# Kernel optimization log

Measured on AMD Instinct MI355X. Metric: run time of the kernel, lower is better.

The kernel has to match this reference:

```python
import jax, jax.numpy as jnp
import numpy as np

B, T, F, U = 64, 512, 1024, 64


def setup_inputs() -> dict:
    key = jax.random.key(0)
    ks = jax.random.split(key, 6)
    return {
        "x": jax.random.normal(ks[0], (B, T, F), dtype=jnp.float32),
        "kernel": jax.random.normal(ks[1], (F, U), dtype=jnp.float32) * (1.0 / np.sqrt(F)),
        "bias": jax.random.normal(ks[2], (U,), dtype=jnp.float32) * 0.02,
        "chain_kernel": jax.random.normal(ks[3], (U, U), dtype=jnp.float32) * 0.1,
        "left_boundary": jax.random.normal(ks[4], (U,), dtype=jnp.float32) * 0.1,
        "right_boundary": jax.random.normal(ks[5], (U,), dtype=jnp.float32) * 0.1,
    }


def _viterbi_decode(potentials, chain_kernel):
    # potentials: [B, T, U], chain_kernel: [U, U]
    def step(alpha, pot_t):
        # alpha: [B, U] best score ending in each tag at t-1
        scores = alpha[:, :, None] + chain_kernel[None, :, :] + pot_t[:, None, :]  # [B, U_prev, U_cur]
        return jnp.max(scores, axis=1), jnp.argmax(scores, axis=1)

    pots_t = jnp.moveaxis(potentials[:, 1:], 1, 0)  # [T-1, B, U]
    alpha_last, backptrs = jax.lax.scan(step, potentials[:, 0], pots_t)
    last_tag = jnp.argmax(alpha_last, axis=-1)  # [B]

    def back(tag, bp):
        prev = jnp.take_along_axis(bp, tag[:, None], axis=1)[:, 0]
        return prev, prev

    _, tags = jax.lax.scan(back, last_tag, backptrs, reverse=True)  # [T-1, B], positions 0..T-2
    path = jnp.concatenate([jnp.moveaxis(tags, 0, 1), last_tag[:, None]], axis=1)
    return path.astype(jnp.int32)


def reference(x, kernel, bias, chain_kernel, left_boundary, right_boundary):
    # dense projection (activation = linear)
    potentials = jnp.einsum("btf,fu->btu", x, kernel) + bias  # [B, T, U]
    # boundary energies (mask=None path: add to first/last timestep)
    potentials = potentials.at[:, 0, :].add(left_boundary)
    potentials = potentials.at[:, -1, :].add(right_boundary)
    return _viterbi_decode(potentials, chain_kernel)
```

## Files before the change

kernel.cpp:

```cpp
#include <hip/hip_runtime.h>

#define B_ 64
#define T_ 512
#define F_ 1024
#define U_ 64
#define FK 128
#define NCH (F_ / FK)

__global__ __launch_bounds__(256, 2) void crf_gemm_kernel(
    const float* __restrict__ x, const float* __restrict__ w,
    const float* __restrict__ bias, const float* __restrict__ lb,
    const float* __restrict__ rb, float* __restrict__ pot)
{
    __shared__ float wlds[FK * U_];

    const int tid = threadIdx.x;
    const int rt = tid >> 4;
    const int ut = tid & 15;
    const int n0 = blockIdx.x * 64;
    const int r0 = rt * 4;
    const int u0 = ut * 4;

    float acc[4][4];
#pragma unroll
    for (int i = 0; i < 4; ++i)
#pragma unroll
        for (int j = 0; j < 4; ++j) acc[i][j] = 0.f;

    const float* xrow = x + (size_t)(n0 + r0) * F_;

    float4 wst[8];
#pragma unroll
    for (int l = 0; l < 8; ++l)
        wst[l] = *reinterpret_cast<const float4*>(w + (size_t)(l * 256 + tid) * 4);
#pragma unroll
    for (int l = 0; l < 8; ++l)
        *reinterpret_cast<float4*>(&wlds[(l * 256 + tid) * 4]) = wst[l];
    __syncthreads();

    float4 xp0[4], xp1[4];
#pragma unroll
    for (int i = 0; i < 4; ++i)
        xp0[i] = *reinterpret_cast<const float4*>(xrow + (size_t)i * F_ + 0);
#pragma unroll
    for (int i = 0; i < 4; ++i)
        xp1[i] = *reinterpret_cast<const float4*>(xrow + (size_t)i * F_ + 4);

    for (int c = 0; c < NCH; ++c) {
        if (c + 1 < NCH) {
#pragma unroll
            for (int l = 0; l < 8; ++l)
                wst[l] = *reinterpret_cast<const float4*>(
                    w + (size_t)(c + 1) * (FK * U_) + (size_t)(l * 256 + tid) * 4);
        }

        float4 wc[4];
#pragma unroll
        for (int j = 0; j < 4; ++j)
            wc[j] = *reinterpret_cast<const float4*>(&wlds[(0 + j) * U_ + u0]);

        for (int kk = 0; kk < FK / 4; ++kk) {
            const int kg = (c * FK + kk * 4 + 8) & (F_ - 1);
            float4 xn[4];
#pragma unroll
            for (int i = 0; i < 4; ++i)
                xn[i] = *reinterpret_cast<const float4*>(xrow + (size_t)i * F_ + kg);

            float4 wn[4];
            const int krn = (kk * 4 + 4) & (FK - 1);
#pragma unroll
            for (int j = 0; j < 4; ++j)
                wn[j] = *reinterpret_cast<const float4*>(&wlds[(krn + j) * U_ + u0]);

#pragma unroll
            for (int ff = 0; ff < 4; ++ff) {
                const float4 wf = wc[ff];
#pragma unroll
                for (int i = 0; i < 4; ++i) {
                    const float xs = (ff == 0) ? xp0[i].x : (ff == 1) ? xp0[i].y
                                   : (ff == 2) ? xp0[i].z : xp0[i].w;
                    acc[i][0] = fmaf(xs, wf.x, acc[i][0]);
                    acc[i][1] = fmaf(xs, wf.y, acc[i][1]);
                    acc[i][2] = fmaf(xs, wf.z, acc[i][2]);
                    acc[i][3] = fmaf(xs, wf.w, acc[i][3]);
                }
            }
#pragma unroll
            for (int i = 0; i < 4; ++i) { xp0[i] = xp1[i]; xp1[i] = xn[i]; }
#pragma unroll
            for (int j = 0; j < 4; ++j) wc[j] = wn[j];
        }

        if (c + 1 < NCH) {
            __syncthreads();
#pragma unroll
            for (int l = 0; l < 8; ++l)
                *reinterpret_cast<float4*>(&wlds[(l * 256 + tid) * 4]) = wst[l];
            __syncthreads();
        }
    }

    const int t0 = n0 & (T_ - 1);
    const float4 bs4 = *reinterpret_cast<const float4*>(bias + u0);
    const float4 lb4 = *reinterpret_cast<const float4*>(lb + u0);
    const float4 rb4 = *reinterpret_cast<const float4*>(rb + u0);

#pragma unroll
    for (int i = 0; i < 4; ++i) {
        const int n = n0 + r0 + i;
        const int t = t0 + r0 + i;
        float4 o;
        o.x = acc[i][0] + bs4.x;
        o.y = acc[i][1] + bs4.y;
        o.z = acc[i][2] + bs4.z;
        o.w = acc[i][3] + bs4.w;
        if (t == 0)      { o.x += lb4.x; o.y += lb4.y; o.z += lb4.z; o.w += lb4.w; }
        if (t == T_ - 1) { o.x += rb4.x; o.y += rb4.y; o.z += rb4.z; o.w += rb4.w; }
        *reinterpret_cast<float4*>(pot + (size_t)n * U_ + u0) = o;
    }
}

__global__ __launch_bounds__(256) void crf_viterbi_kernel(
    const float* __restrict__ pot, const float* __restrict__ chain,
    int* __restrict__ path)
{
    const int b = blockIdx.x;
    const int tid = threadIdx.x;
    const int u = tid & 63;
    const int g = tid >> 6;

    __shared__ __align__(16) float alpha_s[64];
    __shared__ float pval[4][64];
    __shared__ int   pidx[4][64];
    __shared__ unsigned char bp[T_ - 1][64];
    __shared__ unsigned char cmap[4][64];
    __shared__ int es[4];

    float chain_r[16];
#pragma unroll
    for (int k = 0; k < 16; ++k)
        chain_r[k] = chain[(size_t)(g * 16 + k) * U_ + u];

    const float* potb = pot + (size_t)b * T_ * U_;

    if (g == 0) alpha_s[u] = potb[u];
    __syncthreads();

    float pc = potb[(size_t)U_ + u];

    for (int t = 1; t < T_; ++t) {
        const int tn = (t + 1 < T_) ? (t + 1) : (T_ - 1);
        const float pn = potb[(size_t)tn * U_ + u];

        const float4* a4 = reinterpret_cast<const float4*>(alpha_s);
        float best = -3.402823466e38f;
        int bidx = 0;
#pragma unroll
        for (int q = 0; q < 4; ++q) {
            const float4 av = a4[g * 4 + q];
            const float avv[4] = {av.x, av.y, av.z, av.w};
#pragma unroll
            for (int kk = 0; kk < 4; ++kk) {
                const int k = q * 4 + kk;
                const float s2 = (avv[kk] + chain_r[k]) + pc;
                if (s2 > best) { best = s2; bidx = g * 16 + k; }
            }
        }
        pval[g][u] = best;
        pidx[g][u] = bidx;
        __syncthreads();
        if (g == 0) {
            float bv = pval[0][u];
            int   bi = pidx[0][u];
#pragma unroll
            for (int j = 1; j < 4; ++j) {
                const float v = pval[j][u];
                if (v > bv) { bv = v; bi = pidx[j][u]; }
            }
            bp[t - 1][u] = (unsigned char)bi;
            alpha_s[u] = bv;
        }
        __syncthreads();
        pc = pn;
    }

    const int r0c = g * 128;
    const int r1c = (g == 3) ? (T_ - 1) : (g + 1) * 128;

    {
        int tag = u;
        for (int r = r1c - 1; r >= r0c; --r) tag = bp[r][tag];
        cmap[g][u] = (unsigned char)tag;
    }
    __syncthreads();

    if (tid == 0) {
        float bvv = alpha_s[0];
        int bii = 0;
        for (int v = 1; v < 64; ++v) {
            const float a = alpha_s[v];
            if (a > bvv) { bvv = a; bii = v; }
        }
        path[(size_t)b * T_ + (T_ - 1)] = bii;
        const int e3 = bii;
        const int e2 = cmap[3][e3];
        const int e1 = cmap[2][e2];
        const int e0 = cmap[1][e1];
        es[0] = e0; es[1] = e1; es[2] = e2; es[3] = e3;
    }
    __syncthreads();

    if (u == 0) {
        int tag = es[g];
        int* pb = path + (size_t)b * T_;
        for (int r = r1c - 1; r >= r0c; --r) {
            tag = bp[r][tag];
            pb[r] = tag;
        }
    }
}

extern "C" void kernel_launch(void* const* d_in, const int* in_sizes, int n_in,
                              void* d_out, int out_size, void* d_ws, size_t ws_size,
                              hipStream_t stream) {
    const float* x  = (const float*)d_in[0];
    const float* w  = (const float*)d_in[1];
    const float* bs = (const float*)d_in[2];
    const float* ck = (const float*)d_in[3];
    const float* lb = (const float*)d_in[4];
    const float* rb = (const float*)d_in[5];

    float* pot = (float*)d_ws;
    int* path  = (int*)d_out;

    crf_gemm_kernel<<<dim3(B_ * T_ / 64), dim3(256), 0, stream>>>(x, w, bs, lb, rb, pot);
    crf_viterbi_kernel<<<dim3(B_), dim3(256), 0, stream>>>(pot, ck, path);
}
```

Baseline: 344.5 us.

## Fuse projection GEMM into Viterbi kernel with producer waves computing potentials

Replaces the separate GEMM and Viterbi kernels with a single kernel of one 512-thread block per batch element. Four consumer waves run the Viterbi recurrence while four producer waves compute the next 64 timesteps of potentials into a double-buffered LDS tile, interleaved with each step's barriers. The intent is to remove the global round trip of the potentials and the standalone GEMM launch by hiding the projection behind the serial recurrence. In exchange, the GEMM now runs on only 64 blocks with no LDS reuse of the weights, and producer global-load latency can extend each barrier-bound Viterbi step.

Measured after the change: 757.0 us. +119.7%, slower.

```diff
diff --git a/kernel.cpp b/kernel.cpp
--- a/kernel.cpp
+++ b/kernel.cpp
@@ -4,131 +4,22 @@
 #define T_ 512
 #define F_ 1024
 #define U_ 64
-#define FK 128
-#define NCH (F_ / FK)
-
-__global__ __launch_bounds__(256, 2) void crf_gemm_kernel(
+
+__global__ __launch_bounds__(512) void crf_fused_kernel(
     const float* __restrict__ x, const float* __restrict__ w,
-    const float* __restrict__ bias, const float* __restrict__ lb,
-    const float* __restrict__ rb, float* __restrict__ pot)
-{
-    __shared__ float wlds[FK * U_];
-
-    const int tid = threadIdx.x;
-    const int rt = tid >> 4;
-    const int ut = tid & 15;
-    const int n0 = blockIdx.x * 64;
-    const int r0 = rt * 4;
-    const int u0 = ut * 4;
-
-    float acc[4][4];
-#pragma unroll
-    for (int i = 0; i < 4; ++i)
-#pragma unroll
-        for (int j = 0; j < 4; ++j) acc[i][j] = 0.f;
-
-    const float* xrow = x + (size_t)(n0 + r0) * F_;
-
-    float4 wst[8];
-#pragma unroll
-    for (int l = 0; l < 8; ++l)
-        wst[l] = *reinterpret_cast<const float4*>(w + (size_t)(l * 256 + tid) * 4);
-#pragma unroll
-    for (int l = 0; l < 8; ++l)
-        *reinterpret_cast<float4*>(&wlds[(l * 256 + tid) * 4]) = wst[l];
-    __syncthreads();
-
-    float4 xp0[4], xp1[4];
-#pragma unroll
-    for (int i = 0; i < 4; ++i)
-        xp0[i] = *reinterpret_cast<const float4*>(xrow + (size_t)i * F_ + 0);
-#pragma unroll
-    for (int i = 0; i < 4; ++i)
-        xp1[i] = *reinterpret_cast<const float4*>(xrow + (size_t)i * F_ + 4);
-
-    for (int c = 0; c < NCH; ++c) {
-        if (c + 1 < NCH) {
-#pragma unroll
-            for (int l = 0; l < 8; ++l)
-                wst[l] = *reinterpret_cast<const float4*>(
-                    w + (size_t)(c + 1) * (FK * U_) + (size_t)(l * 256 + tid) * 4);
-        }
-
-        float4 wc[4];
-#pragma unroll
-        for (int j = 0; j < 4; ++j)
-            wc[j] = *reinterpret_cast<const float4*>(&wlds[(0 + j) * U_ + u0]);
-
-        for (int kk = 0; kk < FK / 4; ++kk) {
-            const int kg = (c * FK + kk * 4 + 8) & (F_ - 1);
-            float4 xn[4];
-#pragma unroll
-            for (int i = 0; i < 4; ++i)
-                xn[i] = *reinterpret_cast<const float4*>(xrow + (size_t)i * F_ + kg);
-
-            float4 wn[4];
-            const int krn = (kk * 4 + 4) & (FK - 1);
-#pragma unroll
-            for (int j = 0; j < 4; ++j)
-                wn[j] = *reinterpret_cast<const float4*>(&wlds[(krn + j) * U_ + u0]);
-
-#pragma unroll
-            for (int ff = 0; ff < 4; ++ff) {
-                const float4 wf = wc[ff];
-#pragma unroll
-                for (int i = 0; i < 4; ++i) {
-                    const float xs = (ff == 0) ? xp0[i].x : (ff == 1) ? xp0[i].y
-                                   : (ff == 2) ? xp0[i].z : xp0[i].w;
-                    acc[i][0] = fmaf(xs, wf.x, acc[i][0]);
-                    acc[i][1] = fmaf(xs, wf.y, acc[i][1]);
-                    acc[i][2] = fmaf(xs, wf.z, acc[i][2]);
-                    acc[i][3] = fmaf(xs, wf.w, acc[i][3]);
-                }
-            }
-#pragma unroll
-            for (int i = 0; i < 4; ++i) { xp0[i] = xp1[i]; xp1[i] = xn[i]; }
-#pragma unroll
-            for (int j = 0; j < 4; ++j) wc[j] = wn[j];
-        }
-
-        if (c + 1 < NCH) {
-            __syncthreads();
-#pragma unroll
-            for (int l = 0; l < 8; ++l)
-                *reinterpret_cast<float4*>(&wlds[(l * 256 + tid) * 4]) = wst[l];
-            __syncthreads();
-        }
-    }
-
-    const int t0 = n0 & (T_ - 1);
-    const float4 bs4 = *reinterpret_cast<const float4*>(bias + u0);
-    const float4 lb4 = *reinterpret_cast<const float4*>(lb + u0);
-    const float4 rb4 = *reinterpret_cast<const float4*>(rb + u0);
-
-#pragma unroll
-    for (int i = 0; i < 4; ++i) {
-        const int n = n0 + r0 + i;
-        const int t = t0 + r0 + i;
-        float4 o;
-        o.x = acc[i][0] + bs4.x;
-        o.y = acc[i][1] + bs4.y;
-        o.z = acc[i][2] + bs4.z;
-        o.w = acc[i][3] + bs4.w;
-        if (t == 0)      { o.x += lb4.x; o.y += lb4.y; o.z += lb4.z; o.w += lb4.w; }
-        if (t == T_ - 1) { o.x += rb4.x; o.y += rb4.y; o.z += rb4.z; o.w += rb4.w; }
-        *reinterpret_cast<float4*>(pot + (size_t)n * U_ + u0) = o;
-    }
-}
-
-__global__ __launch_bounds__(256) void crf_viterbi_kernel(
-    const float* __restrict__ pot, const float* __restrict__ chain,
+    const float* __restrict__ bias, const float* __restrict__ chain,
+    const float* __restrict__ lb, const float* __restrict__ rb,
     int* __restrict__ path)
 {
     const int b = blockIdx.x;
     const int tid = threadIdx.x;
-    const int u = tid & 63;
-    const int g = tid >> 6;
-
+    const int lane = tid & 63;
+    const int wave = tid >> 6;
+    const bool cons = (wave < 4);
+    const int g = wave & 3;
+    const int u = lane;
+
+    __shared__ __align__(16) float potl[2][64][64];
     __shared__ __align__(16) float alpha_s[64];
     __shared__ float pval[4][64];
     __shared__ int   pidx[4][64];
@@ -136,61 +27,200 @@
     __shared__ unsigned char cmap[4][64];
     __shared__ int es[4];
 
+    {
+        const int rt = tid >> 4;
+        const int u0 = (tid & 15) * 4;
+        float a0[4] = {0.f, 0.f, 0.f, 0.f};
+        float a1[4] = {0.f, 0.f, 0.f, 0.f};
+        const float* xr = x + ((size_t)b * T_ + rt * 2) * F_;
+        for (int k4 = 0; k4 < F_ / 4; ++k4) {
+            const float4 x0 = *reinterpret_cast<const float4*>(xr + k4 * 4);
+            const float4 x1 = *reinterpret_cast<const float4*>(xr + F_ + k4 * 4);
+            const float4 w0 = *reinterpret_cast<const float4*>(w + (size_t)(k4 * 4 + 0) * U_ + u0);
+            const float4 w1 = *reinterpret_cast<const float4*>(w + (size_t)(k4 * 4 + 1) * U_ + u0);
+            const float4 w2 = *reinterpret_cast<const float4*>(w + (size_t)(k4 * 4 + 2) * U_ + u0);
+            const float4 w3 = *reinterpret_cast<const float4*>(w + (size_t)(k4 * 4 + 3) * U_ + u0);
+            a0[0] = fmaf(x0.x, w0.x, a0[0]); a0[1] = fmaf(x0.x, w0.y, a0[1]);
+            a0[2] = fmaf(x0.x, w0.z, a0[2]); a0[3] = fmaf(x0.x, w0.w, a0[3]);
+            a1[0] = fmaf(x1.x, w0.x, a1[0]); a1[1] = fmaf(x1.x, w0.y, a1[1]);
+            a1[2] = fmaf(x1.x, w0.z, a1[2]); a1[3] = fmaf(x1.x, w0.w, a1[3]);
+            a0[0] = fmaf(x0.y, w1.x, a0[0]); a0[1] = fmaf(x0.y, w1.y, a0[1]);
+            a0[2] = fmaf(x0.y, w1.z, a0[2]); a0[3] = fmaf(x0.y, w1.w, a0[3]);
+            a1[0] = fmaf(x1.y, w1.x, a1[0]); a1[1] = fmaf(x1.y, w1.y, a1[1]);
+            a1[2] = fmaf(x1.y, w1.z, a1[2]); a1[3] = fmaf(x1.y, w1.w, a1[3]);
+            a0[0] = fmaf(x0.z, w2.x, a0[0]); a0[1] = fmaf(x0.z, w2.y, a0[1]);
+            a0[2] = fmaf(x0.z, w2.z, a0[2]); a0[3] = fmaf(x0.z, w2.w, a0[3]);
+            a1[0] = fmaf(x1.z, w2.x, a1[0]); a1[1] = fmaf(x1.z, w2.y, a1[1]);
+            a1[2] = fmaf(x1.z, w2.z, a1[2]); a1[3] = fmaf(x1.z, w2.w, a1[3]);
+            a0[0] = fmaf(x0.w, w3.x, a0[0]); a0[1] = fmaf(x0.w, w3.y, a0[1]);
+            a0[2] = fmaf(x0.w, w3.z, a0[2]); a0[3] = fmaf(x0.w, w3.w, a0[3]);
+            a1[0] = fmaf(x1.w, w3.x, a1[0]); a1[1] = fmaf(x1.w, w3.y, a1[1]);
+            a1[2] = fmaf(x1.w, w3.z, a1[2]); a1[3] = fmaf(x1.w, w3.w, a1[3]);
+        }
+        const float4 bs4 = *reinterpret_cast<const float4*>(bias + u0);
+        const float4 lb4 = *reinterpret_cast<const float4*>(lb + u0);
+        {
+            float4 o;
+            o.x = a0[0] + bs4.x; o.y = a0[1] + bs4.y;
+            o.z = a0[2] + bs4.z; o.w = a0[3] + bs4.w;
+            if (rt == 0) { o.x += lb4.x; o.y += lb4.y; o.z += lb4.z; o.w += lb4.w; }
+            *reinterpret_cast<float4*>(&potl[0][rt * 2][u0]) = o;
+        }
+        {
+            float4 o;
+            o.x = a1[0] + bs4.x; o.y = a1[1] + bs4.y;
+            o.z = a1[2] + bs4.z; o.w = a1[3] + bs4.w;
+            *reinterpret_cast<float4*>(&potl[0][rt * 2 + 1][u0]) = o;
+        }
+    }
+
     float chain_r[16];
-#pragma unroll
-    for (int k = 0; k < 16; ++k)
-        chain_r[k] = chain[(size_t)(g * 16 + k) * U_ + u];
-
-    const float* potb = pot + (size_t)b * T_ * U_;
-
-    if (g == 0) alpha_s[u] = potb[u];
-    __syncthreads();
-
-    float pc = potb[(size_t)U_ + u];
+    const int prt = (tid & 255) >> 4;
+    const int pu0 = (tid & 15) * 4;
+    float pacc[4][4];
+
+#define PROD_FMAQ(KQ)                                                         \
+    {                                                                         \
+        _Pragma("unroll")                                                     \
+        for (int i = 0; i < 4; ++i) {                                         \
+            pacc[i][0] = fmaf(xv[KQ][i].x, wv[KQ][0].x, pacc[i][0]);          \
+            pacc[i][1] = fmaf(xv[KQ][i].x, wv[KQ][0].y, pacc[i][1]);          \
+            pacc[i][2] = fmaf(xv[KQ][i].x, wv[KQ][0].z, pacc[i][2]);          \
+            pacc[i][3] = fmaf(xv[KQ][i].x, wv[KQ][0].w, pacc[i][3]);          \
+        }                                                                     \
+        _Pragma("unroll")                                                     \
+        for (int i = 0; i < 4; ++i) {                                         \
+            pacc[i][0] = fmaf(xv[KQ][i].y, wv[KQ][1].x, pacc[i][0]);          \
+            pacc[i][1] = fmaf(xv[KQ][i].y, wv[KQ][1].y, pacc[i][1]);          \
+            pacc[i][2] = fmaf(xv[KQ][i].y, wv[KQ][1].z, pacc[i][2]);          \
+            pacc[i][3] = fmaf(xv[KQ][i].y, wv[KQ][1].w, pacc[i][3]);          \
+        }                                                                     \
+        _Pragma("unroll")                                                     \
+        for (int i = 0; i < 4; ++i) {                                         \
+            pacc[i][0] = fmaf(xv[KQ][i].z, wv[KQ][2].x, pacc[i][0]);          \
+            pacc[i][1] = fmaf(xv[KQ][i].z, wv[KQ][2].y, pacc[i][1]);          \
+            pacc[i][2] = fmaf(xv[KQ][i].z, wv[KQ][2].z, pacc[i][2]);          \
+            pacc[i][3] = fmaf(xv[KQ][i].z, wv[KQ][2].w, pacc[i][3]);          \
+        }                                                                     \
+        _Pragma("unroll")                                                     \
+        for (int i = 0; i < 4; ++i) {                                         \
+            pacc[i][0] = fmaf(xv[KQ][i].w, wv[KQ][3].x, pacc[i][0]);          \
+            pacc[i][1] = fmaf(xv[KQ][i].w, wv[KQ][3].y, pacc[i][1]);          \
+            pacc[i][2] = fmaf(xv[KQ][i].w, wv[KQ][3].z, pacc[i][2]);          \
+            pacc[i][3] = fmaf(xv[KQ][i].w, wv[KQ][3].w, pacc[i][3]);          \
+        }                                                                     \
+    }
+
+    if (cons) {
+#pragma unroll
+        for (int k = 0; k < 16; ++k)
+            chain_r[k] = chain[(size_t)(g * 16 + k) * U_ + u];
+    } else {
+#pragma unroll
+        for (int i = 0; i < 4; ++i)
+#pragma unroll
+            for (int j = 0; j < 4; ++j) pacc[i][j] = 0.f;
+        float4 xv[4][4], wv[4][4];
+        const float* xr = x + ((size_t)b * T_ + 64 + prt * 4) * F_;
+        const float* wr = w + pu0;
+#pragma unroll
+        for (int kq = 0; kq < 4; ++kq) {
+#pragma unroll
+            for (int i = 0; i < 4; ++i)
+                xv[kq][i] = *reinterpret_cast<const float4*>(xr + (size_t)i * F_ + kq * 4);
+#pragma unroll
+            for (int j = 0; j < 4; ++j)
+                wv[kq][j] = *reinterpret_cast<const float4*>(wr + (size_t)(kq * 4 + j) * U_);
+        }
+        PROD_FMAQ(0) PROD_FMAQ(1) PROD_FMAQ(2) PROD_FMAQ(3)
+    }
+    __syncthreads();
+
+    if (cons && g == 0) alpha_s[u] = potl[0][0][u];
+    __syncthreads();
 
     for (int t = 1; t < T_; ++t) {
-        const int tn = (t + 1 < T_) ? (t + 1) : (T_ - 1);
-        const float pn = potb[(size_t)tn * U_ + u];
-
-        const float4* a4 = reinterpret_cast<const float4*>(alpha_s);
-        float best = -3.402823466e38f;
-        int bidx = 0;
-#pragma unroll
-        for (int q = 0; q < 4; ++q) {
-            const float4 av = a4[g * 4 + q];
-            const float avv[4] = {av.x, av.y, av.z, av.w};
-#pragma unroll
-            for (int kk = 0; kk < 4; ++kk) {
-                const int k = q * 4 + kk;
-                const float s2 = (avv[kk] + chain_r[k]) + pc;
-                if (s2 > best) { best = s2; bidx = g * 16 + k; }
-            }
-        }
-        pval[g][u] = best;
-        pidx[g][u] = bidx;
+        const int c = (t >> 6) + 1;
+        const int s = t & 63;
+        float4 xv[4][4], wv[4][4];
+
+        if (cons) {
+            const float pc = potl[(t >> 6) & 1][t & 63][u];
+            const float4* a4 = reinterpret_cast<const float4*>(alpha_s);
+            float best = -3.402823466e38f;
+            int bidx = 0;
+#pragma unroll
+            for (int q = 0; q < 4; ++q) {
+                const float4 av = a4[g * 4 + q];
+                const float avv[4] = {av.x, av.y, av.z, av.w};
+#pragma unroll
+                for (int kk = 0; kk < 4; ++kk) {
+                    const int k = q * 4 + kk;
+                    const float s2 = (avv[kk] + chain_r[k]) + pc;
+                    if (s2 > best) { best = s2; bidx = g * 16 + k; }
+                }
+            }
+            pval[g][u] = best;
+            pidx[g][u] = bidx;
+        } else if (c < 8) {
+            if (s == 0) {
+#pragma unroll
+                for (int i = 0; i < 4; ++i)
+#pragma unroll
+                    for (int j = 0; j < 4; ++j) pacc[i][j] = 0.f;
+            }
+            const float* xr = x + ((size_t)b * T_ + c * 64 + prt * 4) * F_ + s * 16;
+            const float* wr = w + (size_t)(s * 16) * U_ + pu0;
+#pragma unroll
+            for (int kq = 0; kq < 4; ++kq) {
+#pragma unroll
+                for (int i = 0; i < 4; ++i)
+                    xv[kq][i] = *reinterpret_cast<const float4*>(xr + (size_t)i * F_ + kq * 4);
+#pragma unroll
+                for (int j = 0; j < 4; ++j)
+                    wv[kq][j] = *reinterpret_cast<const float4*>(wr + (size_t)(kq * 4 + j) * U_);
+            }
+            PROD_FMAQ(0) PROD_FMAQ(1)
+        }
         __syncthreads();
-        if (g == 0) {
-            float bv = pval[0][u];
-            int   bi = pidx[0][u];
-#pragma unroll
-            for (int j = 1; j < 4; ++j) {
-                const float v = pval[j][u];
-                if (v > bv) { bv = v; bi = pidx[j][u]; }
-            }
-            bp[t - 1][u] = (unsigned char)bi;
-            alpha_s[u] = bv;
+
+        if (cons) {
+            if (g == 0) {
+                float bv = pval[0][u];
+                int   bi = pidx[0][u];
+#pragma unroll
+                for (int j = 1; j < 4; ++j) {
+                    const float v = pval[j][u];
+                    if (v > bv) { bv = v; bi = pidx[j][u]; }
+                }
+                bp[t - 1][u] = (unsigned char)bi;
+                alpha_s[u] = bv;
+            }
+        } else if (c < 8) {
+            PROD_FMAQ(2) PROD_FMAQ(3)
+            if (s == 63) {
+                const float4 bs4 = *reinterpret_cast<const float4*>(bias + pu0);
+                const float4 rb4 = *reinterpret_cast<const float4*>(rb + pu0);
+#pragma unroll
+                for (int i = 0; i < 4; ++i) {
+                    const int row = c * 64 + prt * 4 + i;
+                    float4 o;
+                    o.x = pacc[i][0] + bs4.x; o.y = pacc[i][1] + bs4.y;
+                    o.z = pacc[i][2] + bs4.z; o.w = pacc[i][3] + bs4.w;
+                    if (row == T_ - 1) { o.x += rb4.x; o.y += rb4.y; o.z += rb4.z; o.w += rb4.w; }
+                    *reinterpret_cast<float4*>(&potl[c & 1][row & 63][pu0]) = o;
+                }
+            }
         }
         __syncthreads();
-        pc = pn;
-    }
-
-    const int r0c = g * 128;
-    const int r1c = (g == 3) ? (T_ - 1) : (g + 1) * 128;
-
-    {
-        int tag = u;
+    }
+
+    if (cons) {
+        const int r0c = g * 128;
+        const int r1c = (g == 3) ? (T_ - 1) : (g + 1) * 128;
+        int tag = lane;
         for (int r = r1c - 1; r >= r0c; --r) tag = bp[r][tag];
-        cmap[g][u] = (unsigned char)tag;
+        cmap[g][lane] = (unsigned char)tag;
     }
     __syncthreads();
 
@@ -210,7 +240,9 @@
     }
     __syncthreads();
 
-    if (u == 0) {
+    if (cons && lane == 0) {
+        const int r0c = g * 128;
+        const int r1c = (g == 3) ? (T_ - 1) : (g + 1) * 128;
         int tag = es[g];
         int* pb = path + (size_t)b * T_;
         for (int r = r1c - 1; r >= r0c; --r) {
@@ -218,6 +250,7 @@
             pb[r] = tag;
         }
     }
+#undef PROD_FMAQ
 }
 
 extern "C" void kernel_launch(void* const* d_in, const int* in_sizes, int n_in,
@@ -229,10 +262,7 @@
     const float* ck = (const float*)d_in[3];
     const float* lb = (const float*)d_in[4];
     const float* rb = (const float*)d_in[5];
-
-    float* pot = (float*)d_ws;
-    int* path  = (int*)d_out;
-
-    crf_gemm_kernel<<<dim3(B_ * T_ / 64), dim3(256), 0, stream>>>(x, w, bs, lb, rb, pot);
-    crf_viterbi_kernel<<<dim3(B_), dim3(256), 0, stream>>>(pot, ck, path);
+    int* path = (int*)d_out;
+
+    crf_fused_kernel<<<dim3(B_), dim3(512), 0, stream>>>(x, w, bs, ck, lb, rb, path);
 }
```
